# Performance work log

Hardware: AMD Instinct MI355X
Metric: run time of the kernel (lower is better)

## Reference

```python
import jax, jax.numpy as jnp
import numpy as np

HEADS, DIM_HEAD, BITS = 12, 64, 4


def quantize(q, bits):
    # per-tensor affine fake-quant, exactly as the torch quantize()
    s = (q.max() - q.min()) / (2.0 ** bits - 1.0)
    z = jnp.round(2.0 ** bits - 1.0 - q.max() / s)
    return jnp.round(q / s + z), s, z


def setup_inputs() -> dict:
    key = jax.random.key(0)
    k1, k2, k3, k4 = jax.random.split(key, 4)
    return {
        "x": jax.random.normal(k1, (4, 1024, 768), jnp.float32),
        "w_qkv": jax.random.normal(k2, (2304, 768), jnp.float32) * 0.02,  # torch Linear weight [out,in]
        "w_out": jax.random.normal(k3, (768, 768), jnp.float32) * 0.02,
        "b_out": jax.random.normal(k4, (768,), jnp.float32) * 0.02,
    }


def reference(x, w_qkv, w_out, b_out):
    scale = DIM_HEAD ** -0.5
    B, N, D = x.shape
    # --- quantized QKV projection: x @ W^T with zero-point correction ---
    xq, sx1, zx1 = quantize(x, BITS)
    w1, sw1, zw1 = quantize(w_qkv.T, BITS)  # [D, 3*inner]
    xqkv = (xq @ w1
            - w1.sum(0, keepdims=True) * zx1
            - xq.sum(2, keepdims=True) * zw1
            + zx1 * zw1 * D) * (sx1 * sw1)  # [B, N, 3*inner]
    q, k, v = jnp.split(xqkv, 3, axis=-1)
    to_heads = lambda t: t.reshape(B, N, HEADS, DIM_HEAD).transpose(0, 2, 1, 3)  # b h n d
    q, k, v = to_heads(q), to_heads(k), to_heads(v)
    # --- quantized QK^T (note: original omits the +zq*zk*d term) ---
    qq, sq, zq = quantize(q, BITS)
    kq, sk, zk = quantize(k.transpose(0, 1, 3, 2), BITS)  # b h d n
    dots = (qq @ kq
            - kq.sum(2, keepdims=True) * zq
            - qq.sum(3, keepdims=True) * zk) * (scale * sq * sk)  # b h n n
    a = jax.nn.softmax(dots, axis=-1)
    # --- quantized A @ V ---
    aq, sa, za = quantize(a, BITS)
    vq, sv, zv = quantize(v, BITS)
    out = (aq @ vq
           - vq.sum(2, keepdims=True) * za
           - aq.sum(3, keepdims=True) * zv
           + za * zv * N) * (sa * sv)  # b h n d
    out = out.transpose(0, 2, 1, 3).reshape(B, N, HEADS * DIM_HEAD)
    # --- quantized output projection (faithful to original: correction uses
    # xqkv.sum / xqkv width, reproducing the source's use of `x` here) ---
    oq, sx2, zx2 = quantize(out, BITS)
    w2, sw2, zw2 = quantize(w_out.T, BITS)  # [inner, D]
    o = (oq @ w2
         - w2.sum(0, keepdims=True) * zx2
         - xqkv.sum(2, keepdims=True) * zw2
         + zx2 * zw2 * xqkv.shape[2]) * (sx2 * sw2) + b_out
    return o
```

## Files before the change

### kernel.cpp

```cpp
#include <hip/hip_runtime.h>
#include <math.h>

#define HEADS 12
#define DH    64
#define Dm    768
#define I3    2304
#define Nn    1024
#define Mm    4096
#define BHt   48
#define LOG2E 1.4426950408889634f

#define P_X  0
#define P_W1 1
#define P_Q  2
#define P_K  3
#define P_V  4
#define P_A  5
#define P_O  6
#define P_W2 7

typedef int v4i __attribute__((ext_vector_type(4)));

#if __has_builtin(__builtin_amdgcn_exp2f)
#define EXP2(x) __builtin_amdgcn_exp2f(x)
#else
#define EXP2(x) exp2f(x)
#endif

__device__ inline unsigned encf(float f) {
    unsigned u = __float_as_uint(f);
    return (u & 0x80000000u) ? ~u : (u | 0x80000000u);
}
__device__ inline float decf(unsigned u) {
    return (u & 0x80000000u) ? __uint_as_float(u & 0x7fffffffu) : __uint_as_float(~u);
}
__device__ inline void get_sz(const unsigned* scal, int pair, float* s, float* z) {
    float mn = decf(scal[2 * pair]);
    float mx = decf(scal[2 * pair + 1]);
    float ss = (mx - mn) / 15.0f;
    *s = ss;
    *z = rintf(15.0f - mx / ss);
}

__global__ __launch_bounds__(256) void k_init(unsigned* scal, float* z1, int n1, float* z2, int n2) {
    int g = blockIdx.x * 256 + threadIdx.x;
    if (g < n1) z1[g] = 0.f;
    if (g < n2) z2[g] = 0.f;
    if (g < 8) { scal[2 * g] = 0xFFFFFFFFu; scal[2 * g + 1] = 0u; }
}

__global__ __launch_bounds__(256) void k_minmax3(const float* x, const float* w1, const float* w2,
                                                 unsigned* scal) {
    __shared__ float rmn[256], rmx[256];
    int bid = blockIdx.x, tid = threadIdx.x;
    const float* src; int rows, pair, b0, nb;
    if (bid < 256)      { src = x;  rows = 4096; pair = P_X;  b0 = 0;   nb = 256; }
    else if (bid < 384) { src = w1; rows = 2304; pair = P_W1; b0 = 256; nb = 128; }
    else                { src = w2; rows = 768;  pair = P_W2; b0 = 384; nb = 64;  }
    float mn = INFINITY, mx = -INFINITY;
    for (int r = bid - b0; r < rows; r += nb) {
        const float* row = src + (long)r * 768;
#pragma unroll
        for (int k = 0; k < 3; ++k) {
            float v = row[tid + k * 256];
            mn = fminf(mn, v); mx = fmaxf(mx, v);
        }
    }
    rmn[tid] = mn; rmx[tid] = mx; __syncthreads();
    for (int s = 128; s > 0; s >>= 1) {
        if (tid < s) { rmn[tid] = fminf(rmn[tid], rmn[tid + s]); rmx[tid] = fmaxf(rmx[tid], rmx[tid + s]); }
        __syncthreads();
    }
    if (tid == 0) {
        atomicMin(&scal[2 * pair], encf(rmn[0]));
        atomicMax(&scal[2 * pair + 1], encf(rmx[0]));
    }
}

__global__ __launch_bounds__(256) void k_quant3(const float* x, const float* w1, const float* w2,
                                                const unsigned* scal,
                                                signed char* xq, signed char* wq, signed char* w2q,
                                                float* rs_x, float* rs_w1, float* rs_w2) {
    __shared__ float red[256];
    int bid = blockIdx.x, tid = threadIdx.x;
    const float* src; signed char* dq; float* rs; int pair, r;
    if (bid < 4096)      { src = x;  dq = xq;  rs = rs_x;  pair = P_X;  r = bid; }
    else if (bid < 6400) { src = w1; dq = wq;  rs = rs_w1; pair = P_W1; r = bid - 4096; }
    else                 { src = w2; dq = w2q; rs = rs_w2; pair = P_W2; r = bid - 6400; }
    float s, z; get_sz(scal, pair, &s, &z);
    const float* row = src + (long)r * 768;
    signed char* drow = dq + (long)r * 768;
    float acc = 0.f;
#pragma unroll
    for (int k = 0; k < 3; ++k) {
        int c = tid + k * 256;
        float q = rintf(row[c] / s + z);
        drow[c] = (signed char)(int)q;
        acc += q;
    }
    red[tid] = acc; __syncthreads();
    for (int s2 = 128; s2 > 0; s2 >>= 1) { if (tid < s2) red[tid] += red[tid + s2]; __syncthreads(); }
    if (tid == 0) rs[r] = red[0];
}

__global__ __launch_bounds__(256) void k_quant_rows(const float* src, const unsigned* scal, int pair,
                                                    signed char* dq) {
    int r = blockIdx.x, tid = threadIdx.x;
    float s, z; get_sz(scal, pair, &s, &z);
    const float* row = src + (long)r * 768;
    signed char* drow = dq + (long)r * 768;
#pragma unroll
    for (int k = 0; k < 3; ++k) {
        int c = tid + k * 256;
        float q = rintf(row[c] / s + z);
        drow[c] = (signed char)(int)q;
    }
}

__global__ __launch_bounds__(256) void k_gemm_mfma(const signed char* A, const signed char* B,
                                                   const float* colsumB, const float* rowsumA,
                                                   const float* bias, float* C, int K, int ldC,
                                                   const unsigned* scal, int pairA, int pairB,
                                                   float corrK, int do_stats, float* rowsum_out,
                                                   unsigned* scal_mm) {
    __shared__ __align__(16) signed char As[128 * 64];
    __shared__ __align__(16) signed char Bs[128 * 64];
    __shared__ float red[256];
    int tid = threadIdx.x;
    int wave = tid >> 6, lane = tid & 63;
    int col16 = lane & 15, quad = lane >> 4;
    long rowbase = (long)blockIdx.y * 128;
    long colbase = (long)blockIdx.x * 128;

    int c4 = tid & 3, r4 = tid >> 2;
    const signed char* ag0 = A + (rowbase + r4) * K + c4 * 16;
    const signed char* ag1 = A + (rowbase + r4 + 64) * K + c4 * 16;
    const signed char* bg0 = B + (colbase + r4) * K + c4 * 16;
    const signed char* bg1 = B + (colbase + r4 + 64) * K + c4 * 16;
    int soff0 = ((r4 >> 4) << 10) + (c4 << 8) + ((r4 & 15) << 4);
    int soff1 = soff0 + 4096;

    v4i ra0 = *(const v4i*)ag0;
    v4i ra1 = *(const v4i*)ag1;
    v4i rb0 = *(const v4i*)bg0;
    v4i rb1 = *(const v4i*)bg1;

    const int afrag_off = wave * 2048 + quad * 256 + col16 * 16;
    const int bfrag_off = quad * 256 + col16 * 16;
    v4i acc[2][8] = {};
    int nk = K >> 6;
    for (int kt = 0; kt < nk; ++kt) {
        *(v4i*)(As + soff0) = ra0;
        *(v4i*)(As + soff1) = ra1;
        *(v4i*)(Bs + soff0) = rb0;
        *(v4i*)(Bs + soff1) = rb1;
        __syncthreads();
        if (kt + 1 < nk) {
            int ko = (kt + 1) << 6;
            ra0 = *(const v4i*)(ag0 + ko);
            ra1 = *(const v4i*)(ag1 + ko);
            rb0 = *(const v4i*)(bg0 + ko);
            rb1 = *(const v4i*)(bg1 + ko);
        }
        v4i af0 = *(const v4i*)(As + afrag_off);
        v4i af1 = *(const v4i*)(As + afrag_off + 1024);
        v4i bf[8];
#pragma unroll
        for (int g = 0; g < 8; ++g) bf[g] = *(const v4i*)(Bs + bfrag_off + g * 1024);
#pragma unroll
        for (int g = 0; g < 8; ++g) {
            acc[0][g] = __builtin_amdgcn_mfma_i32_16x16x64_i8(af0, bf[g], acc[0][g], 0, 0, 0);
            acc[1][g] = __builtin_amdgcn_mfma_i32_16x16x64_i8(af1, bf[g], acc[1][g], 0, 0, 0);
        }
        __syncthreads();
    }

    float sA, zA, sB, zB;
    get_sz(scal, pairA, &sA, &zA);
    get_sz(scal, pairB, &sB, &zB);
    float sAB = sA * sB;
    float zz = (zA * zB) * corrK;
    float vmn = INFINITY, vmx = -INFINITY;
    float rowpart[2][4] = {};
#pragma unroll
    for (int i2 = 0; i2 < 2; ++i2)
#pragma unroll
        for (int g = 0; g < 8; ++g) {
            long col = colbase + g * 16 + col16;
            float cs = colsumB[col] * zA;
            float bv = bias ? bias[col] : 0.f;
#pragma unroll
            for (int r = 0; r < 4; ++r) {
                long row = rowbase + wave * 32 + i2 * 16 + quad * 4 + r;
                float v = ((float)acc[i2][g][r] - cs - rowsumA[row] * zB + zz) * sAB + bv;
                C[row * ldC + col] = v;
                rowpart[i2][r] += v;
                vmn = fminf(vmn, v); vmx = fmaxf(vmx, v);
            }
        }
    if (do_stats) {
#pragma unroll
        for (int i2 = 0; i2 < 2; ++i2)
#pragma unroll
            for (int r = 0; r < 4; ++r) {
                float s = rowpart[i2][r];
                s += __shfl_xor(s, 1); s += __shfl_xor(s, 2);
                s += __shfl_xor(s, 4); s += __shfl_xor(s, 8);
                if (col16 == 0)
                    atomicAdd(&rowsum_out[rowbase + wave * 32 + i2 * 16 + quad * 4 + r], s);
            }
        int pair = P_Q + (int)(colbase / 768);
        red[tid] = vmx; __syncthreads();
        for (int s = 128; s > 0; s >>= 1) { if (tid < s) red[tid] = fmaxf(red[tid], red[tid + s]); __syncthreads(); }
        if (tid == 0) atomicMax(&scal_mm[2 * pair + 1], encf(red[0]));
        __syncthreads();
        red[tid] = vmn; __syncthreads();
        for (int s = 128; s > 0; s >>= 1) { if (tid < s) red[tid] = fminf(red[tid], red[tid + s]); __syncthreads(); }
        if (tid == 0) atomicMin(&scal_mm[2 * pair], encf(red[0]));
    }
}

__global__ __launch_bounds__(256) void k_quant_qkv2(const float* xqkv, const unsigned* scal,
                                                    signed char* qq, signed char* kq, signed char* vqT,
                                                    float* rowsum_qq, float* cskc, float* colsum_vq) {
    __shared__ __align__(16) signed char vt[64 * 80];
    __shared__ float vred[4][64];
    int blk = blockIdx.x;
    int bh = blk >> 4, itile = blk & 15;
    int tid = threadIdx.x;
    int wave = tid >> 6, d = tid & 63;
    int b = bh / HEADS, h = bh - HEADS * b;
    float sq, zq, sk, zk, sv, zv;
    get_sz(scal, P_Q, &sq, &zq);
    get_sz(scal, P_K, &sk, &zk);
    get_sz(scal, P_V, &sv, &zv);
    float zqcsc2 = zq * ((0.125f * sq) * sk) * LOG2E;
    int vb = 0;
    float vsum = 0.f;
    for (int ir = 0; ir < 16; ++ir) {
        int il = wave * 16 + ir;
        int i = itile * 64 + il;
        const float* row = xqkv + ((long)b * Nn + i) * I3 + h * DH;
        float q = rintf(row[d] / sq + zq);
        float k = rintf(row[768 + d] / sk + zk);
        float v = rintf(row[1536 + d] / sv + zv);
        long o = ((long)bh * Nn + i) * 64 + d;
        qq[o] = (signed char)(int)q;
        kq[o] = (signed char)(int)k;
        vsum += v;
        vb |= ((int)v & 0xff) << ((ir & 3) * 8);
        if ((ir & 3) == 3) {
            *(int*)(vt + d * 80 + (il & ~3)) = vb;
            vb = 0;
        }
        float s1 = q, s2 = k;
        for (int off = 32; off > 0; off >>= 1) {
            s1 += __shfl_down(s1, off);
            s2 += __shfl_down(s2, off);
        }
        if (d == 0) { rowsum_qq[bh * Nn + i] = s1; cskc[bh * Nn + i] = s2 * zqcsc2; }
    }
    vred[wave][d] = vsum;
    __syncthreads();
    int dd = tid >> 2, c = tid & 3;
    *(v4i*)(vqT + ((long)bh * 64 + dd) * 1024 + itile * 64 + c * 16) = *(const v4i*)(vt + dd * 80 + c * 16);
    if (tid < 64)
        atomicAdd(&colsum_vq[bh * 64 + tid],
                  ((vred[0][tid] + vred[1][tid]) + vred[2][tid]) + vred[3][tid]);
}

__global__ __launch_bounds__(256) void k_attn_a8(const signed char* qq, const signed char* kq,
                                                 const float* rowsum_qq, const float* cskc,
                                                 unsigned* scal, float* rowmax, float* sumexp) {
    __shared__ float red[256];
    int blk = blockIdx.x;
    int bh = blk >> 4, itile = blk & 15;
    int tid = threadIdx.x;
    int wave = tid >> 6, lane = tid & 63;
    int col16 = lane & 15, quad = lane >> 4;
    int rowbase = itile * 64 + wave * 16;
    const signed char* kbase = kq + (long)bh * Nn * 64;
    const float* ck = cskc + bh * Nn;
    v4i afrag = *(const v4i*)(qq + ((long)bh * Nn + rowbase + col16) * 64 + quad * 16);
    float sq, zq, sk, zk;
    get_sz(scal, P_Q, &sq, &zq);
    get_sz(scal, P_K, &sk, &zk);
    float csc2 = ((0.125f * sq) * sk) * LOG2E;
    float rzc[4];
#pragma unroll
    for (int r = 0; r < 4; ++r)
        rzc[r] = rowsum_qq[bh * Nn + rowbase + quad * 4 + r] * zk * csc2;
    v4i zero = {0, 0, 0, 0};
    float m[4]    = {-INFINITY, -INFINITY, -INFINITY, -INFINITY};
    float se[4]   = {0.f, 0.f, 0.f, 0.f};
    float lmin[4] = {INFINITY, INFINITY, INFINITY, INFINITY};
    const signed char* kf = kbase + (long)col16 * 64 + quad * 16;
    v4i kb[2][4];
#pragma unroll
    for (int t = 0; t < 4; ++t) kb[0][t] = *(const v4i*)(kf + (long)(t * 16) * 64);
#pragma unroll 2
    for (int ch = 0; ch < 16; ++ch) {
        int cur = ch & 1, nxt = cur ^ 1;
        int pch = (ch < 15) ? ch + 1 : 15;
#pragma unroll
        for (int t = 0; t < 4; ++t)
            kb[nxt][t] = *(const v4i*)(kf + (long)(pch * 64 + t * 16) * 64);
#pragma unroll
        for (int t = 0; t < 4; ++t) {
            v4i d = __builtin_amdgcn_mfma_i32_16x16x64_i8(afrag, kb[cur][t], zero, 0, 0, 0);
            float ckv = ck[ch * 64 + t * 16 + col16];
#pragma unroll
            for (int r = 0; r < 4; ++r) {
                float dv = fmaf((float)d[r], csc2, -(ckv + rzc[r]));
                lmin[r] = fminf(lmin[r], dv);
                float mn = fmaxf(m[r], dv);
                se[r] = fmaf(se[r], EXP2(m[r] - mn), EXP2(dv - mn));
                m[r] = mn;
            }
        }
    }
#pragma unroll
    for (int r = 0; r < 4; ++r) {
#pragma unroll
        for (int off = 1; off < 16; off <<= 1) {
            float mo = __shfl_xor(m[r], off);
            float so = __shfl_xor(se[r], off);
            float mino = __shfl_xor(lmin[r], off);
            float mn = fmaxf(m[r], mo);
            se[r] = fmaf(se[r], EXP2(m[r] - mn), so * EXP2(mo - mn));
            m[r] = mn;
            lmin[r] = fminf(lmin[r], mino);
        }
    }
    float amax_c = -INFINITY, amin_c = INFINITY;
    if (col16 == 0) {
#pragma unroll
        for (int r = 0; r < 4; ++r) {
            int grow = bh * Nn + rowbase + quad * 4 + r;
            rowmax[grow] = m[r];
            sumexp[grow] = se[r];
            amax_c = fmaxf(amax_c, 1.0f / se[r]);
            amin_c = fminf(amin_c, EXP2(lmin[r] - m[r]) / se[r]);
        }
    }
    red[tid] = amax_c; __syncthreads();
    for (int s = 128; s > 0; s >>= 1) { if (tid < s) red[tid] = fmaxf(red[tid], red[tid + s]); __syncthreads(); }
    if (tid == 0) atomicMax(&scal[2 * P_A + 1], encf(red[0]));
    __syncthreads();
    red[tid] = amin_c; __syncthreads();
    for (int s = 128; s > 0; s >>= 1) { if (tid < s) red[tid] = fminf(red[tid], red[tid + s]); __syncthreads(); }
    if (tid == 0) atomicMin(&scal[2 * P_A], encf(red[0]));
}

__global__ __launch_bounds__(256) void k_attn_b8(const signed char* qq, const signed char* kq,
                                                 const signed char* vqT, const float* rowsum_qq,
                                                 const float* cskc, const float* colsum_vq,
                                                 const float* rowmax, const float* sumexp,
                                                 unsigned* scal, float* out_mat) {
    __shared__ __align__(16) signed char AqB[8192];
    __shared__ float red[256];
    int blk = blockIdx.x;
    int bh = blk >> 4, itile = blk & 15;
    int tid = threadIdx.x;
    int wave = tid >> 6, lane = tid & 63;
    int col16 = lane & 15, quad = lane >> 4;
    int rowbase = itile * 64 + wave * 16;
    int b = bh / HEADS, h = bh - HEADS * b;
    const signed char* kbase = kq + (long)bh * Nn * 64;
    const signed char* vbase = vqT + (long)bh * 64 * 1024;
    const float* ck = cskc + bh * Nn;
    v4i afrag = *(const v4i*)(qq + ((long)bh * Nn + rowbase + col16) * 64 + quad * 16);
    float sq, zq, sk, zk, sv, zv, sa, za;
    get_sz(scal, P_Q, &sq, &zq);
    get_sz(scal, P_K, &sk, &zk);
    get_sz(scal, P_V, &sv, &zv);
    get_sz(scal, P_A, &sa, &za);
    float csc2 = ((0.125f * sq) * sk) * LOG2E;
    float roff[4], crcp[4];
#pragma unroll
    for (int r = 0; r < 4; ++r) {
        int row = bh * Nn + rowbase + quad * 4 + r;
        roff[r] = rowsum_qq[row] * zk * csc2 + rowmax[row];
        crcp[r] = 1.0f / (sumexp[row] * sa);
    }
    v4i accPV[4] = {};
    float rs_a[4] = {0.f, 0.f, 0.f, 0.f};
    v4i zero = {0, 0, 0, 0};

#define QUANT_CHUNK(CH, BUF)                                                            \
    {                                                                                   \
        signed char* myAq = AqB + (BUF) * 4096 + wave * 1024;                           \
        _Pragma("unroll")                                                               \
        for (int t = 0; t < 4; ++t) {                                                   \
            int jt = (CH) * 4 + t;                                                      \
            v4i bfrag = *(const v4i*)(kbase + (long)(jt * 16 + col16) * 64 + quad * 16);\
            v4i d = __builtin_amdgcn_mfma_i32_16x16x64_i8(afrag, bfrag, zero, 0, 0, 0); \
            float ckv = ck[jt * 16 + col16];                                            \
            _Pragma("unroll")                                                           \
            for (int r = 0; r < 4; ++r) {                                               \
                float es = fmaf((float)d[r], csc2, -(ckv + roff[r]));                   \
                float fastv = fmaf(EXP2(es), crcp[r], za);                              \
                float aqv = rintf(fastv);                                               \
                rs_a[r] += aqv;                                                         \
                myAq[(quad * 4 + r) * 64 + t * 16 + col16] = (signed char)(int)aqv;     \
            }                                                                           \
        }                                                                               \
    }

    QUANT_CHUNK(0, 0)
    for (int ch = 0; ch < 16; ++ch) {
        int cur = ch & 1;
        v4i pa = *(const v4i*)(AqB + cur * 4096 + wave * 1024 + col16 * 64 + quad * 16);
        v4i bv[4];
#pragma unroll
        for (int g = 0; g < 4; ++g)
            bv[g] = *(const v4i*)(vbase + (long)(g * 16 + col16) * 1024 + ch * 64 + quad * 16);
        if (ch < 15) QUANT_CHUNK(ch + 1, cur ^ 1)
#pragma unroll
        for (int g = 0; g < 4; ++g)
            accPV[g] = __builtin_amdgcn_mfma_i32_16x16x64_i8(pa, bv[g], accPV[g], 0, 0, 0);
    }
#undef QUANT_CHUNK

#pragma unroll
    for (int r = 0; r < 4; ++r)
        for (int off = 1; off < 16; off <<= 1) rs_a[r] += __shfl_xor(rs_a[r], off);
    float sav = sa * sv;
    float zz = (za * zv) * 1024.0f;
    float vmn = INFINITY, vmx = -INFINITY;
#pragma unroll
    for (int g = 0; g < 4; ++g) {
        int d = g * 16 + col16;
        float cs = colsum_vq[bh * 64 + d] * za;
#pragma unroll
        for (int r = 0; r < 4; ++r) {
            int i = rowbase + quad * 4 + r;
            float v = ((float)accPV[g][r] - cs - rs_a[r] * zv + zz) * sav;
            out_mat[((long)b * Nn + i) * Dm + h * DH + d] = v;
            vmn = fminf(vmn, v); vmx = fmaxf(vmx, v);
        }
    }
    red[tid] = vmx; __syncthreads();
    for (int s = 128; s > 0; s >>= 1) { if (tid < s) red[tid] = fmaxf(red[tid], red[tid + s]); __syncthreads(); }
    if (tid == 0) atomicMax(&scal[2 * P_O + 1], encf(red[0]));
    __syncthreads();
    red[tid] = vmn; __syncthreads();
    for (int s = 128; s > 0; s >>= 1) { if (tid < s) red[tid] = fminf(red[tid], red[tid + s]); __syncthreads(); }
    if (tid == 0) atomicMin(&scal[2 * P_O], encf(red[0]));
}

extern "C" void kernel_launch(void* const* d_in, const int* in_sizes, int n_in,
                              void* d_out, int out_size, void* d_ws, size_t ws_size,
                              hipStream_t stream) {
    const float* x     = (const float*)d_in[0];
    const float* w_qkv = (const float*)d_in[1];
    const float* w_out = (const float*)d_in[2];
    const float* b_out = (const float*)d_in[3];

    char* ws = (char*)d_ws;
    size_t off = 0;
    auto alloc = [&](size_t n) -> char* {
        char* p = ws + off;
        off = (off + n + 255) & ~(size_t)255;
        return p;
    };
    unsigned*    scal        = (unsigned*)alloc(64);
    float*       xqkv        = (float*)alloc((size_t)Mm * I3 * 4);
    float*       out_mat     = (float*)alloc((size_t)Mm * Dm * 4);
    signed char* xq          = (signed char*)alloc((size_t)Mm * Dm);
    signed char* wq          = (signed char*)alloc((size_t)I3 * Dm);
    signed char* w2q         = (signed char*)alloc((size_t)Dm * Dm);
    signed char* oq          = (signed char*)alloc((size_t)Mm * Dm);
    signed char* qq          = (signed char*)alloc((size_t)BHt * Nn * DH);
    signed char* kq          = (signed char*)alloc((size_t)BHt * Nn * DH);
    signed char* vqT         = (signed char*)alloc((size_t)BHt * Nn * DH);
    float*       rowsum_xq   = (float*)alloc((size_t)Mm * 4);
    float*       colsum_w1   = (float*)alloc((size_t)I3 * 4);
    float*       colsum_w2   = (float*)alloc((size_t)Dm * 4);
    float*       rowsum_xqkv = (float*)alloc((size_t)Mm * 4);
    float*       rowsum_qq   = (float*)alloc((size_t)BHt * Nn * 4);
    float*       cskc        = (float*)alloc((size_t)BHt * Nn * 4);
    float*       colsum_vq   = (float*)alloc((size_t)BHt * DH * 4);
    float*       rowmax      = (float*)alloc((size_t)BHt * Nn * 4);
    float*       sumexp      = (float*)alloc((size_t)BHt * Nn * 4);

    k_init<<<28, 256, 0, stream>>>(scal, rowsum_xqkv, Mm, colsum_vq, BHt * DH);

    k_minmax3<<<448, 256, 0, stream>>>(x, w_qkv, w_out, scal);
    k_quant3<<<7168, 256, 0, stream>>>(x, w_qkv, w_out, scal, xq, wq, w2q,
                                       rowsum_xq, colsum_w1, colsum_w2);

    {
        dim3 g(I3 / 128, Mm / 128);
        k_gemm_mfma<<<g, 256, 0, stream>>>(xq, wq, colsum_w1, rowsum_xq, nullptr, xqkv,
                                           Dm, I3, scal, P_X, P_W1, 768.0f,
                                           1, rowsum_xqkv, scal);
    }

    k_quant_qkv2<<<BHt * 16, 256, 0, stream>>>(xqkv, scal, qq, kq, vqT,
                                               rowsum_qq, cskc, colsum_vq);

    k_attn_a8<<<BHt * 16, 256, 0, stream>>>(qq, kq, rowsum_qq, cskc, scal, rowmax, sumexp);
    k_attn_b8<<<BHt * 16, 256, 0, stream>>>(qq, kq, vqT, rowsum_qq, cskc, colsum_vq,
                                            rowmax, sumexp, scal, out_mat);

    k_quant_rows<<<Mm, 256, 0, stream>>>(out_mat, scal, P_O, oq);

    {
        dim3 g(Dm / 128, Mm / 128);
        k_gemm_mfma<<<g, 256, 0, stream>>>(oq, w2q, colsum_w2, rowsum_xqkv, b_out, (float*)d_out,
                                           Dm, Dm, scal, P_O, P_W2, 2304.0f,
                                           0, nullptr, nullptr);
    }
}
```

Measured before the change: 259.7 us.

## Prefetch K fragments and column sums, swizzle LDS Aq tile, cheaper online softmax

The stats kernel now prefetches the column-sum correction values one chunk ahead alongside the K fragments. Its online-softmax update computes a single exp2 per element instead of two, using a select on whether the new value exceeds the running max. The A·V kernel restructures its loop into a manually double-buffered pipeline that loads K fragments and column sums two chunks ahead, so the QK recompute no longer waits on global loads. It also XOR-swizzles the LDS layout of the quantized attention tile to reduce bank conflicts on the fragment read-back, at the cost of more registers held live.

New measurement: 255.6 us. Within noise of the previous version (-1.6%).

```diff
diff --git a/kernel.cpp b/kernel.cpp
--- a/kernel.cpp
+++ b/kernel.cpp
@@ -295,29 +295,39 @@
     float se[4]   = {0.f, 0.f, 0.f, 0.f};
     float lmin[4] = {INFINITY, INFINITY, INFINITY, INFINITY};
     const signed char* kf = kbase + (long)col16 * 64 + quad * 16;
+    const float* ckp = ck + col16;
     v4i kb[2][4];
-#pragma unroll
-    for (int t = 0; t < 4; ++t) kb[0][t] = *(const v4i*)(kf + (long)(t * 16) * 64);
+    float ckc[4], ckn[4];
+#pragma unroll
+    for (int t = 0; t < 4; ++t) {
+        kb[0][t] = *(const v4i*)(kf + (long)(t * 16) * 64);
+        ckc[t] = ckp[t * 16];
+    }
 #pragma unroll 2
     for (int ch = 0; ch < 16; ++ch) {
         int cur = ch & 1, nxt = cur ^ 1;
         int pch = (ch < 15) ? ch + 1 : 15;
 #pragma unroll
-        for (int t = 0; t < 4; ++t)
+        for (int t = 0; t < 4; ++t) {
             kb[nxt][t] = *(const v4i*)(kf + (long)(pch * 64 + t * 16) * 64);
+            ckn[t] = ckp[pch * 64 + t * 16];
+        }
 #pragma unroll
         for (int t = 0; t < 4; ++t) {
             v4i d = __builtin_amdgcn_mfma_i32_16x16x64_i8(afrag, kb[cur][t], zero, 0, 0, 0);
-            float ckv = ck[ch * 64 + t * 16 + col16];
+            float ckv = ckc[t];
 #pragma unroll
             for (int r = 0; r < 4; ++r) {
                 float dv = fmaf((float)d[r], csc2, -(ckv + rzc[r]));
                 lmin[r] = fminf(lmin[r], dv);
                 float mn = fmaxf(m[r], dv);
-                se[r] = fmaf(se[r], EXP2(m[r] - mn), EXP2(dv - mn));
+                float e = EXP2(fminf(m[r], dv) - mn);
+                se[r] = (dv > m[r]) ? fmaf(se[r], e, 1.0f) : (se[r] + e);
                 m[r] = mn;
             }
         }
+#pragma unroll
+        for (int t = 0; t < 4; ++t) ckc[t] = ckn[t];
     }
 #pragma unroll
     for (int r = 0; r < 4; ++r) {
@@ -386,40 +396,66 @@
     v4i accPV[4] = {};
     float rs_a[4] = {0.f, 0.f, 0.f, 0.f};
     v4i zero = {0, 0, 0, 0};
-
-#define QUANT_CHUNK(CH, BUF)                                                            \
+    const signed char* kf = kbase + (long)col16 * 64 + quad * 16;
+    const float* ckp = ck + col16;
+    const int pa_off = wave * 1024 + col16 * 64 + ((quad ^ (col16 >> 2)) << 4);
+
+    v4i kb0[4], kb1[4];
+    float ckr0[4], ckr1[4];
+#pragma unroll
+    for (int t = 0; t < 4; ++t) {
+        kb0[t] = *(const v4i*)(kf + (long)(t * 16) * 64);
+        ckr0[t] = ckp[t * 16];
+        kb1[t] = *(const v4i*)(kf + (long)(64 + t * 16) * 64);
+        ckr1[t] = ckp[64 + t * 16];
+    }
+
+#define QUANT_CHUNK(BUF, KB, CKR)                                                       \
     {                                                                                   \
         signed char* myAq = AqB + (BUF) * 4096 + wave * 1024;                           \
         _Pragma("unroll")                                                               \
         for (int t = 0; t < 4; ++t) {                                                   \
-            int jt = (CH) * 4 + t;                                                      \
-            v4i bfrag = *(const v4i*)(kbase + (long)(jt * 16 + col16) * 64 + quad * 16);\
-            v4i d = __builtin_amdgcn_mfma_i32_16x16x64_i8(afrag, bfrag, zero, 0, 0, 0); \
-            float ckv = ck[jt * 16 + col16];                                            \
+            v4i d = __builtin_amdgcn_mfma_i32_16x16x64_i8(afrag, KB[t], zero, 0, 0, 0); \
+            float ckv = CKR[t];                                                         \
+            int cswz = ((t ^ quad) << 4) + col16;                                       \
             _Pragma("unroll")                                                           \
             for (int r = 0; r < 4; ++r) {                                               \
                 float es = fmaf((float)d[r], csc2, -(ckv + roff[r]));                   \
                 float fastv = fmaf(EXP2(es), crcp[r], za);                              \
                 float aqv = rintf(fastv);                                               \
                 rs_a[r] += aqv;                                                         \
-                myAq[(quad * 4 + r) * 64 + t * 16 + col16] = (signed char)(int)aqv;     \
+                myAq[(quad * 4 + r) * 64 + cswz] = (signed char)(int)aqv;               \
             }                                                                           \
         }                                                                               \
     }
 
-    QUANT_CHUNK(0, 0)
-    for (int ch = 0; ch < 16; ++ch) {
-        int cur = ch & 1;
-        v4i pa = *(const v4i*)(AqB + cur * 4096 + wave * 1024 + col16 * 64 + quad * 16);
-        v4i bv[4];
-#pragma unroll
-        for (int g = 0; g < 4; ++g)
-            bv[g] = *(const v4i*)(vbase + (long)(g * 16 + col16) * 1024 + ch * 64 + quad * 16);
-        if (ch < 15) QUANT_CHUNK(ch + 1, cur ^ 1)
-#pragma unroll
-        for (int g = 0; g < 4; ++g)
-            accPV[g] = __builtin_amdgcn_mfma_i32_16x16x64_i8(pa, bv[g], accPV[g], 0, 0, 0);
-    }
+#define BODY(CH, CUR, KBc, CKc, KBn, CKn)                                               \
+    {                                                                                   \
+        v4i pa = *(const v4i*)(AqB + (CUR) * 4096 + pa_off);                            \
+        v4i bv[4];                                                                      \
+        _Pragma("unroll")                                                               \
+        for (int g = 0; g < 4; ++g)                                                     \
+            bv[g] = *(const v4i*)(vbase + (long)(g * 16 + col16) * 1024 + (CH) * 64 + quad * 16); \
+        if ((CH) < 14) {                                                                \
+            _Pragma("unroll")                                                           \
+            for (int t = 0; t < 4; ++t) {                                               \
+                KBc[t] = *(const v4i*)(kf + (long)(((CH) + 2) * 64 + t * 16) * 64);     \
+                CKc[t] = ckp[((CH) + 2) * 64 + t * 16];                                 \
+            }                                                                           \
+        }                                                                               \
+        if ((CH) < 15) QUANT_CHUNK(1 - (CUR), KBn, CKn)                                 \
+        _Pragma("unroll")                                                               \
+        for (int g = 0; g < 4; ++g)                                                     \
+            accPV[g] = __builtin_amdgcn_mfma_i32_16x16x64_i8(pa, bv[g], accPV[g], 0, 0, 0); \
+    }
+
+    QUANT_CHUNK(0, kb0, ckr0)
+    for (int ch2 = 0; ch2 < 8; ++ch2) {
+        int ch = ch2 * 2;
+        BODY(ch, 0, kb0, ckr0, kb1, ckr1)
+        BODY(ch + 1, 1, kb1, ckr1, kb0, ckr0)
+    }
+#undef BODY
 #undef QUANT_CHUNK
 
 #pragma unroll
```
